# Performance work log

Measured on AMD Instinct MI355X. Metric: run time of the kernel, lower is better.

The kernel has to match this reference:

```python
import jax, jax.numpy as jnp
import numpy as np
from jax.scipy.special import logsumexp

B, T, D = 256, 2048, 64


def setup_inputs() -> dict:
    key = jax.random.key(0)
    k1, k2, k3, k4 = jax.random.split(key, 4)
    p = jax.random.normal(k1, (B, T, D), dtype=jnp.float32)
    labels = jax.random.randint(k2, (B, T), 0, D)
    y = jax.nn.one_hot(labels, D, dtype=jnp.int32)  # [B,T,D] one-hot labels
    # valid lengths in [T//2, T]; mask == 1 marks padding positions
    lengths = jax.random.randint(k3, (B,), T // 2, T + 1)
    mask = (jnp.arange(T)[None, :] >= lengths[:, None]).astype(jnp.int32)
    transition = 0.1 * jax.random.normal(k4, (D, D), dtype=jnp.float32)
    return {"p": p, "y": y, "mask": mask, "transition": transition}


def reference(p, y, mask, transition):
    # CRF negative log-likelihood per example: logZ - emission_score - transition_score
    Bb = p.shape[0]
    valid = (1 - mask).astype(jnp.float32)            # [B,T], 1 = valid token
    y1 = y.astype(jnp.float32) * valid[:, :, None]    # masked one-hot labels
    s1 = jnp.sum(y1 * p, axis=(1, 2))                 # emission score
    pair = jnp.einsum('btd,bte->bde', y1[:, :-1], y1[:, 1:])  # label bigram counts
    s2 = jnp.sum(pair * transition, axis=(1, 2))      # transition score

    # forward algorithm: alpha_t = p_t + logsumexp(alpha_{t-1}[:, :, None] + T)
    def step(state, inp):
        new = inp + logsumexp(state[:, :, None] + transition[None, :, :], axis=1)
        return new, new

    xs = jnp.moveaxis(p[:, 1:, :], 1, 0)              # [T-1, B, D]
    _, a1 = jax.lax.scan(step, p[:, 0, :], xs)        # a1: [T-1, B, D]

    # index of alpha at the last valid timestep (length L -> a1 index L-2)
    m1 = jnp.argmin(
        jnp.concatenate([valid.astype(jnp.int32), jnp.zeros((Bb, 1), jnp.int32)], axis=1),
        axis=1) - 2                                   # [B]
    last = a1[m1, jnp.arange(Bb)]                     # [B, D]
    logZ = logsumexp(last, axis=-1)
    return logZ - s1 - s2
```

## Files before the change

### kernel.cpp

```cpp
#include <hip/hip_runtime.h>
#include <stdint.h>
#include <string.h>

#define BB 256
#define TT 2048
#define DD 64
#define CC 64
#define SS 32
#define C_L2E 1.44269504f
#define C_LN2 0.69314718f
#define C_BIAS 0.0028174f

typedef short sh8  __attribute__((ext_vector_type(8)));
typedef float f32x4 __attribute__((ext_vector_type(4)));

union BU { sh8 v8; unsigned int u[4]; unsigned short s[8]; };

__device__ __forceinline__ float expf_fast(float x) { return __builtin_amdgcn_exp2f(x * C_L2E); }
__device__ __forceinline__ unsigned short bf16rne(float x) {
    unsigned int u = __float_as_uint(x);
    u += 0x7FFF + ((u >> 16) & 1u);
    return (unsigned short)(u >> 16);
}
__device__ __forceinline__ unsigned int pkbf(float hi, float lo) {
    return __builtin_amdgcn_perm(__float_as_uint(hi), __float_as_uint(lo), 0x07060302u);
}

#define DPPMAX(x, ctrl, rm, bm) { int _xi = __float_as_int(x);                              \
    int _yi = __builtin_amdgcn_update_dpp(_xi, _xi, ctrl, rm, bm, false);                   \
    x = fmaxf(x, __int_as_float(_yi)); }

__global__ __launch_bounds__(256) void crf_score(
    const float* __restrict__ p, const int* __restrict__ y,
    const int* __restrict__ mask, const float* __restrict__ tr,
    float* __restrict__ wsS, int* __restrict__ wsL)
{
    __shared__ int mk[257];
    __shared__ unsigned char labs[257];
    __shared__ float redf[4];
    __shared__ int redi[4];
    const int c = blockIdx.y, t0 = blockIdx.x * 256;
    const int tid = threadIdx.x;
    const int g = tid & 15, sub = tid >> 4;
    const size_t cb = (size_t)c * TT;

    mk[tid] = mask[cb + t0 + tid];
    if (tid == 0) mk[256] = (t0 + 256 < TT) ? mask[cb + t0 + 256] : 1;
    __syncthreads();

    float s1 = 0.f;
    int vc = 0;
#pragma unroll
    for (int k = 0; k < 16; ++k) {
        const int ti = k * 16 + sub;
        if (mk[ti] == 0) {
            int4 v = ((const int4*)y)[(cb + t0 + ti) * 16 + g];
            int cand = v.w ? 4 * g + 3 : v.z ? 4 * g + 2 : v.y ? 4 * g + 1 : v.x ? 4 * g : -1;
#pragma unroll
            for (int xm = 1; xm <= 8; xm <<= 1) {
                int o = __shfl_xor(cand, xm, 16);
                cand = o > cand ? o : cand;
            }
            if (g == 0) {
                labs[ti] = (unsigned char)cand;
                s1 += p[(cb + t0 + ti) * DD + cand];
                vc += 1;
            }
        }
    }
    if (tid < 16 && mk[256] == 0) {
        int4 v = ((const int4*)y)[(cb + t0 + 256) * 16 + tid];
        int cand = v.w ? 4 * tid + 3 : v.z ? 4 * tid + 2 : v.y ? 4 * tid + 1 : v.x ? 4 * tid : -1;
#pragma unroll
        for (int xm = 1; xm <= 8; xm <<= 1) {
            int o = __shfl_xor(cand, xm, 16);
            cand = o > cand ? o : cand;
        }
        if (tid == 0) labs[256] = (unsigned char)cand;
    }
    __syncthreads();

    float s2 = 0.f;
    if (mk[tid + 1] == 0)
        s2 = tr[(int)labs[tid] * DD + (int)labs[tid + 1]];

    float acc = s1 + s2;
#pragma unroll
    for (int xm = 32; xm >= 1; xm >>= 1) { acc += __shfl_xor(acc, xm, 64); vc += __shfl_xor(vc, xm, 64); }
    if ((tid & 63) == 0) { redf[tid >> 6] = acc; redi[tid >> 6] = vc; }
    __syncthreads();
    if (tid == 0) {
        atomicAdd(&wsS[c], redf[0] + redf[1] + redf[2] + redf[3]);
        atomicAdd(&wsL[c], redi[0] + redi[1] + redi[2] + redi[3]);
    }
}

__global__ __launch_bounds__(256) void crf_probe(
    const float* __restrict__ p, const float* __restrict__ tr,
    const int* __restrict__ wsL,
    unsigned short* __restrict__ wsA, unsigned short* __restrict__ wsB, int* __restrict__ wsSig)
{
    const int tid = threadIdx.x, w = tid >> 6, lane = tid & 63;
    const int q = lane >> 4, ml = lane & 15;
    const int cg = blockIdx.x;
    const int ic = blockIdx.y * 2 + (w >> 1);
    const int bwd = w & 1;
    const int c = cg * 16 + ml;
    const int Lml = wsL[c];
    const int t0 = ic * SS, t1 = t0 + SS;
    const int ts = (ic == 0) ? 1 : t0;
    const float* prow = p + (size_t)c * TT * DD;

    BU A[4][2];
#pragma unroll
    for (int mt = 0; mt < 4; ++mt)
#pragma unroll
        for (int kt2 = 0; kt2 < 2; ++kt2)
#pragma unroll
            for (int j = 0; j < 8; ++j) {
                int lam = 32 * kt2 + 16 * (j >> 2) + 4 * q + (j & 3);
                float tv = bwd ? tr[(16 * mt + ml) * DD + lam] : tr[lam * DD + 16 * mt + ml];
                A[mt][kt2].s[j] = (short)bf16rne(expf_fast(tv));
            }

    float xs[16];
    if (!bwd && ic == 0) {
#pragma unroll
        for (int k = 0; k < 4; ++k) {
            f32x4 v = *(const f32x4*)(prow + 16 * k + 4 * q);
#pragma unroll
            for (int r = 0; r < 4; ++r)
                xs[(k >> 1) * 8 + (k & 1) * 4 + r] = __builtin_amdgcn_exp2f(fmaf(v[r], C_L2E, C_BIAS));
        }
    } else {
#pragma unroll
        for (int i = 0; i < 16; ++i) xs[i] = 1.0f;
    }

    int mL = Lml;
#pragma unroll
    for (int xm = 32; xm >= 1; xm >>= 1) { int o = __shfl_xor(mL, xm, 64); mL = o > mL ? o : mL; }
    int ibeg = 0, iend = SS;
    if (!bwd) { int ir = mL - t0; if (ir < 0) ir = 0; iend = (ir + 3) & ~3; if (iend > SS) iend = SS; }
    else      { int ir = t1 - mL; if (ir < 0) ir = 0; ibeg = ir & ~3; if (ibeg > SS) ibeg = SS; }

    int sig = 0;
    const f32x4 z4 = {0.f, 0.f, 0.f, 0.f};

    if (ibeg < iend) {
        f32x4 er[4][4];
#pragma unroll
        for (int s = 0; s < 4; ++s) {
            int i = ibeg + s;
            int t = bwd ? (t1 - 1 - i) : (t0 + i);
#pragma unroll
            for (int k = 0; k < 4; ++k)
                er[s][k] = *(const f32x4*)(prow + (size_t)t * DD + 16 * k + 4 * q);
        }
        for (int ib = ibeg; ib < iend; ib += 4) {
#pragma unroll
            for (int s = 0; s < 4; ++s) {
                const int i = ib + s;
                const int t = bwd ? (t1 - 1 - i) : (t0 + i);
                const bool act = (t >= ts) && (t < Lml);
                float ee[4][4];
#pragma unroll
                for (int k = 0; k < 4; ++k)
#pragma unroll
                    for (int r = 0; r < 4; ++r)
                        ee[k][r] = __builtin_amdgcn_exp2f(fmaf(er[s][k][r], C_L2E, C_BIAS));
                {
                    int ipf = i + 4;
                    int tpf = bwd ? (t1 - 1 - ipf) : (t0 + ipf);
                    if (tpf < t0) tpf = t0;
                    if (tpf > t1 - 1) tpf = t1 - 1;
#pragma unroll
                    for (int k = 0; k < 4; ++k)
                        er[s][k] = *(const f32x4*)(prow + (size_t)tpf * DD + 16 * k + 4 * q);
                }
                float cand[16];
                BU Bf[2];
                f32x4 acc[4];
                if (!bwd) {
#pragma unroll
                    for (int kt2 = 0; kt2 < 2; ++kt2)
#pragma unroll
                        for (int jj = 0; jj < 4; ++jj)
                            Bf[kt2].u[jj] = pkbf(xs[kt2 * 8 + 2 * jj + 1], xs[kt2 * 8 + 2 * jj]);
#pragma unroll
                    for (int mt = 0; mt < 4; ++mt) {
                        acc[mt] = __builtin_amdgcn_mfma_f32_16x16x32_bf16(A[mt][0].v8, Bf[0].v8, z4, 0, 0, 0);
                        acc[mt] = __builtin_amdgcn_mfma_f32_16x16x32_bf16(A[mt][1].v8, Bf[1].v8, acc[mt], 0, 0, 0);
                    }
#pragma unroll
                    for (int mt = 0; mt < 4; ++mt)
#pragma unroll
                        for (int r = 0; r < 4; ++r)
                            cand[(mt >> 1) * 8 + (mt & 1) * 4 + r] = acc[mt][r] * ee[mt][r];
                } else {
                    float xsc[16];
#pragma unroll
                    for (int kt2 = 0; kt2 < 2; ++kt2)
#pragma unroll
                        for (int h = 0; h < 2; ++h)
#pragma unroll
                            for (int r = 0; r < 4; ++r)
                                xsc[kt2 * 8 + h * 4 + r] = xs[kt2 * 8 + h * 4 + r] * ee[2 * kt2 + h][r];
#pragma unroll
                    for (int kt2 = 0; kt2 < 2; ++kt2)
#pragma unroll
                        for (int jj = 0; jj < 4; ++jj)
                            Bf[kt2].u[jj] = pkbf(xsc[kt2 * 8 + 2 * jj + 1], xsc[kt2 * 8 + 2 * jj]);
#pragma unroll
                    for (int mt = 0; mt < 4; ++mt) {
                        acc[mt] = __builtin_amdgcn_mfma_f32_16x16x32_bf16(A[mt][0].v8, Bf[0].v8, z4, 0, 0, 0);
                        acc[mt] = __builtin_amdgcn_mfma_f32_16x16x32_bf16(A[mt][1].v8, Bf[1].v8, acc[mt], 0, 0, 0);
                    }
#pragma unroll
                    for (int mt = 0; mt < 4; ++mt)
#pragma unroll
                        for (int r = 0; r < 4; ++r)
                            cand[(mt >> 1) * 8 + (mt & 1) * 4 + r] = acc[mt][r];
                }
                if (s == 3) {
                    float mx = fabsf(cand[0]);
#pragma unroll
                    for (int i2 = 1; i2 < 16; ++i2) mx = fmaxf(mx, fabsf(cand[i2]));
                    DPPMAX(mx, 0x111, 0xF, 0xF); DPPMAX(mx, 0x112, 0xF, 0xF);
                    DPPMAX(mx, 0x114, 0xF, 0xF); DPPMAX(mx, 0x118, 0xF, 0xF);
                    DPPMAX(mx, 0x142, 0xA, 0xF); DPPMAX(mx, 0x143, 0xC, 0xF);
                    int smx = __builtin_amdgcn_readlane(__float_as_int(mx), 63);
                    int kk = ((smx >> 23) & 255) - 127;
                    kk = kk < -124 ? -124 : (kk > 124 ? 124 : kk);
                    float sc = __int_as_float((unsigned)(127 - kk) << 23);
#pragma unroll
                    for (int i2 = 0; i2 < 16; ++i2) cand[i2] *= sc;
                    if (act) sig += kk;
                }
#pragma unroll
                for (int i2 = 0; i2 < 16; ++i2) xs[i2] = act ? cand[i2] : xs[i2];
            }
        }
    }

    unsigned short* dst = (bwd ? wsB : wsA) + ((size_t)c * CC + ic) * 64;
#pragma unroll
    for (int kt2 = 0; kt2 < 2; ++kt2)
#pragma unroll
        for (int h = 0; h < 2; ++h)
#pragma unroll
            for (int r = 0; r < 4; ++r)
                dst[32 * kt2 + 16 * h + 4 * q + r] = bf16rne(xs[kt2 * 8 + h * 4 + r]);
    if (!bwd && q == 0) wsSig[c * CC + ic] = sig;
}

__global__ __launch_bounds__(256) void crf_combine(
    const unsigned short* __restrict__ wsA, const unsigned short* __restrict__ wsB,
    const int* __restrict__ wsSig, const float* __restrict__ wsS,
    float* __restrict__ out)
{
    __shared__ float eParts[4];
    const int tid = threadIdx.x, w = tid >> 6, lane = tid & 63;
    const int c = blockIdx.x;

    float Ep = 0.f;
#pragma unroll
    for (int k = 0; k < 16; ++k) {
        const int i = w * 16 + k;
        if (i == 0) continue;
        float b  = __uint_as_float((unsigned)wsB[((size_t)c * CC + i) * 64 + lane] << 16);
        float ap = __uint_as_float((unsigned)wsA[((size_t)c * CC + i - 1) * 64 + lane] << 16);
        float d1 = b * ap, d0 = b;
#pragma unroll
        for (int xm = 32; xm >= 1; xm >>= 1) { d1 += __shfl_xor(d1, xm, 64); d0 += __shfl_xor(d0, xm, 64); }
        Ep += (float)wsSig[c * CC + i] + __builtin_amdgcn_logf(d1) - __builtin_amdgcn_logf(d0);
    }
    if (w == 0) Ep += (float)wsSig[c * CC];
    if (w == 3) {
        float al = __uint_as_float((unsigned)wsA[((size_t)c * CC + CC - 1) * 64 + lane] << 16);
#pragma unroll
        for (int xm = 32; xm >= 1; xm >>= 1) al += __shfl_xor(al, xm, 64);
        Ep += __builtin_amdgcn_logf(al);
    }
    if (lane == 0) eParts[w] = Ep;
    __syncthreads();
    if (tid == 0) {
        float E = eParts[0] + eParts[1] + eParts[2] + eParts[3];
        out[c] = C_LN2 * E - wsS[c];
    }
}

extern "C" void kernel_launch(void* const* d_in, const int* in_sizes, int n_in,
                              void* d_out, int out_size, void* d_ws, size_t ws_size,
                              hipStream_t stream) {
    const float* p  = (const float*)d_in[0];
    const int*   y  = (const int*)d_in[1];
    const int*   mk = (const int*)d_in[2];
    const float* tr = (const float*)d_in[3];
    float* out = (float*)d_out;

    float* wsS  = (float*)d_ws;
    int*   wsL  = (int*)((char*)d_ws + 1024);
    int*   wsSg = (int*)((char*)d_ws + 2048);
    unsigned short* wsA = (unsigned short*)((char*)d_ws + 131072);
    unsigned short* wsB = (unsigned short*)((char*)d_ws + 131072 + (2u << 20));

    hipMemsetAsync(d_ws, 0, 2048, stream);
    crf_score<<<dim3(8, BB), dim3(256), 0, stream>>>(p, y, mk, tr, wsS, wsL);
    crf_probe<<<dim3(16, CC / 2), dim3(256), 0, stream>>>(p, tr, wsL, wsA, wsB, wsSg);
    crf_combine<<<dim3(BB), dim3(256), 0, stream>>>(wsA, wsB, wsSg, wsS, out);
}
```

Baseline: 317.5 us.

## Stage chunk emissions into LDS via direct global-to-LDS loads; halve chunk length

The probe kernel now copies each chunk's emission rows for its 16 sequences into LDS up front with global_load_lds (XOR-swizzled). Both the forward and backward waves then read from LDS instead of issuing per-step global prefetches. Chunks shrink from 32 to 16 steps, doubling the chunk count to 128, and each 128-thread block handles one chunk with a fwd/bwd wave pair. This shortens each wave's serial dependency chain and adds parallelism, at the cost of 64KB LDS per block (limiting occupancy) and twice as many partial vectors for the combine kernel.

Result: slower. 337.1 us (+6.2%).

```diff
diff --git a/kernel.cpp b/kernel.cpp
--- a/kernel.cpp
+++ b/kernel.cpp
@@ -5,8 +5,8 @@
 #define BB 256
 #define TT 2048
 #define DD 64
-#define CC 64
-#define SS 32
+#define CC 128
+#define SS 16
 #define C_L2E 1.44269504f
 #define C_LN2 0.69314718f
 #define C_BIAS 0.0028174f
@@ -24,6 +24,11 @@
 }
 __device__ __forceinline__ unsigned int pkbf(float hi, float lo) {
     return __builtin_amdgcn_perm(__float_as_uint(hi), __float_as_uint(lo), 0x07060302u);
+}
+__device__ __forceinline__ void gl_lds16(void* l, const void* g) {
+    __builtin_amdgcn_global_load_lds(
+        (const __attribute__((address_space(1))) unsigned int*)g,
+        (__attribute__((address_space(3))) unsigned int*)l, 16, 0, 0);
 }
 
 #define DPPMAX(x, ctrl, rm, bm) { int _xi = __float_as_int(x);                              \
@@ -95,22 +100,45 @@
     }
 }
 
-__global__ __launch_bounds__(256) void crf_probe(
+__global__ __launch_bounds__(128) void crf_probe(
     const float* __restrict__ p, const float* __restrict__ tr,
     const int* __restrict__ wsL,
     unsigned short* __restrict__ wsA, unsigned short* __restrict__ wsB, int* __restrict__ wsSig)
 {
+    __shared__ char lds[SS * 4096];
     const int tid = threadIdx.x, w = tid >> 6, lane = tid & 63;
     const int q = lane >> 4, ml = lane & 15;
     const int cg = blockIdx.x;
-    const int ic = blockIdx.y * 2 + (w >> 1);
-    const int bwd = w & 1;
+    const int ic = blockIdx.y;
+    const int bwd = w;
     const int c = cg * 16 + ml;
     const int Lml = wsL[c];
     const int t0 = ic * SS, t1 = t0 + SS;
     const int ts = (ic == 0) ? 1 : t0;
     const float* prow = p + (size_t)c * TT * DD;
 
+    int mL = Lml;
+#pragma unroll
+    for (int xm = 32; xm >= 1; xm >>= 1) { int o = __shfl_xor(mL, xm, 64); mL = o > mL ? o : mL; }
+
+    {
+        const int mls = lane >> 2, u = lane & 3;
+        const int gs = (mls >> 1) & 3;
+        const char* gbase = (const char*)(p + (size_t)(cg * 16 + mls) * TT * DD);
+        const int lofs = (u ^ gs) << 4;
+#pragma unroll
+        for (int s = 0; s < 8; ++s) {
+            const int tt = w * 8 + s;
+            if (t0 + tt < mL) {
+                const char* gsrc = gbase + (size_t)(t0 + tt) * 256 + lofs;
+                char* ldst = lds + tt * 4096;
+#pragma unroll
+                for (int k = 0; k < 4; ++k)
+                    gl_lds16(ldst + k * 1024, gsrc + k * 64);
+            }
+        }
+    }
+
     BU A[4][2];
 #pragma unroll
     for (int mt = 0; mt < 4; ++mt)
@@ -137,47 +165,34 @@
         for (int i = 0; i < 16; ++i) xs[i] = 1.0f;
     }
 
-    int mL = Lml;
-#pragma unroll
-    for (int xm = 32; xm >= 1; xm >>= 1) { int o = __shfl_xor(mL, xm, 64); mL = o > mL ? o : mL; }
     int ibeg = 0, iend = SS;
     if (!bwd) { int ir = mL - t0; if (ir < 0) ir = 0; iend = (ir + 3) & ~3; if (iend > SS) iend = SS; }
     else      { int ir = t1 - mL; if (ir < 0) ir = 0; ibeg = ir & ~3; if (ibeg > SS) ibeg = SS; }
 
+    __syncthreads();
+
     int sig = 0;
     const f32x4 z4 = {0.f, 0.f, 0.f, 0.f};
 
     if (ibeg < iend) {
-        f32x4 er[4][4];
-#pragma unroll
-        for (int s = 0; s < 4; ++s) {
-            int i = ibeg + s;
-            int t = bwd ? (t1 - 1 - i) : (t0 + i);
-#pragma unroll
-            for (int k = 0; k < 4; ++k)
-                er[s][k] = *(const f32x4*)(prow + (size_t)t * DD + 16 * k + 4 * q);
-        }
+        const char* rbase = lds + ml * 64 + ((q ^ ((ml >> 1) & 3)) << 4);
         for (int ib = ibeg; ib < iend; ib += 4) {
 #pragma unroll
             for (int s = 0; s < 4; ++s) {
                 const int i = ib + s;
                 const int t = bwd ? (t1 - 1 - i) : (t0 + i);
+                const int tt = t - t0;
                 const bool act = (t >= ts) && (t < Lml);
+                f32x4 er[4];
+#pragma unroll
+                for (int k = 0; k < 4; ++k)
+                    er[k] = *(const f32x4*)(rbase + tt * 4096 + k * 1024);
                 float ee[4][4];
 #pragma unroll
                 for (int k = 0; k < 4; ++k)
 #pragma unroll
                     for (int r = 0; r < 4; ++r)
-                        ee[k][r] = __builtin_amdgcn_exp2f(fmaf(er[s][k][r], C_L2E, C_BIAS));
-                {
-                    int ipf = i + 4;
-                    int tpf = bwd ? (t1 - 1 - ipf) : (t0 + ipf);
-                    if (tpf < t0) tpf = t0;
-                    if (tpf > t1 - 1) tpf = t1 - 1;
-#pragma unroll
-                    for (int k = 0; k < 4; ++k)
-                        er[s][k] = *(const f32x4*)(prow + (size_t)tpf * DD + 16 * k + 4 * q);
-                }
+                        ee[k][r] = __builtin_amdgcn_exp2f(fmaf(er[k][r], C_L2E, C_BIAS));
                 float cand[16];
                 BU Bf[2];
                 f32x4 acc[4];
@@ -264,9 +279,9 @@
     const int c = blockIdx.x;
 
     float Ep = 0.f;
-#pragma unroll
-    for (int k = 0; k < 16; ++k) {
-        const int i = w * 16 + k;
+#pragma unroll 4
+    for (int k = 0; k < 32; ++k) {
+        const int i = w * 32 + k;
         if (i == 0) continue;
         float b  = __uint_as_float((unsigned)wsB[((size_t)c * CC + i) * 64 + lane] << 16);
         float ap = __uint_as_float((unsigned)wsA[((size_t)c * CC + i - 1) * 64 + lane] << 16);
@@ -301,12 +316,12 @@
 
     float* wsS  = (float*)d_ws;
     int*   wsL  = (int*)((char*)d_ws + 1024);
-    int*   wsSg = (int*)((char*)d_ws + 2048);
-    unsigned short* wsA = (unsigned short*)((char*)d_ws + 131072);
-    unsigned short* wsB = (unsigned short*)((char*)d_ws + 131072 + (2u << 20));
+    int*   wsSg = (int*)((char*)d_ws + 4096);
+    unsigned short* wsA = (unsigned short*)((char*)d_ws + (1u << 18));
+    unsigned short* wsB = (unsigned short*)((char*)d_ws + (1u << 18) + (4u << 20));
 
     hipMemsetAsync(d_ws, 0, 2048, stream);
     crf_score<<<dim3(8, BB), dim3(256), 0, stream>>>(p, y, mk, tr, wsS, wsL);
-    crf_probe<<<dim3(16, CC / 2), dim3(256), 0, stream>>>(p, tr, wsL, wsA, wsB, wsSg);
+    crf_probe<<<dim3(16, CC), dim3(128), 0, stream>>>(p, tr, wsL, wsA, wsB, wsSg);
     crf_combine<<<dim3(BB), dim3(256), 0, stream>>>(wsA, wsB, wsSg, wsS, out);
 }
```

## Split length computation into tiny kernel and co-schedule scoring with forward probe

Applied to the files above, without the earlier changes.

Adds a small kernel that computes each sequence's valid length directly from the mask. The emission/transition scoring and the chunked forward/backward probe then run as one merged launch, with the first 512 blocks doing the probe and the remaining blocks doing the scoring. The intent is to overlap the memory-bound scoring of y and p with the MFMA-bound probe, so the probe no longer waits on the full scoring pass. The cost is one extra tiny launch and a larger merged kernel, whose register usage is set by the heavier probe branch.

Measured after the change: 370.8 us. +16.8%, slower.

```diff
diff --git a/kernel.cpp b/kernel.cpp
--- a/kernel.cpp
+++ b/kernel.cpp
@@ -30,228 +30,239 @@
     int _yi = __builtin_amdgcn_update_dpp(_xi, _xi, ctrl, rm, bm, false);                   \
     x = fmaxf(x, __int_as_float(_yi)); }
 
-__global__ __launch_bounds__(256) void crf_score(
+__global__ __launch_bounds__(256) void crf_len(
+    const int* __restrict__ mask, int* __restrict__ wsL)
+{
+    __shared__ int r4[4];
+    const int c = blockIdx.x, tid = threadIdx.x;
+    const int4* mrow = (const int4*)(mask + (size_t)c * TT);
+    int4 a = mrow[tid * 2], b = mrow[tid * 2 + 1];
+    int s = a.x + a.y + a.z + a.w + b.x + b.y + b.z + b.w;
+#pragma unroll
+    for (int xm = 32; xm >= 1; xm >>= 1) s += __shfl_xor(s, xm, 64);
+    if ((tid & 63) == 0) r4[tid >> 6] = s;
+    __syncthreads();
+    if (tid == 0) wsL[c] = TT - (r4[0] + r4[1] + r4[2] + r4[3]);
+}
+
+__global__ __launch_bounds__(256) void crf_main(
     const float* __restrict__ p, const int* __restrict__ y,
     const int* __restrict__ mask, const float* __restrict__ tr,
-    float* __restrict__ wsS, int* __restrict__ wsL)
+    const int* __restrict__ wsL, float* __restrict__ wsS,
+    unsigned short* __restrict__ wsA, unsigned short* __restrict__ wsB, int* __restrict__ wsSig)
 {
     __shared__ int mk[257];
     __shared__ unsigned char labs[257];
     __shared__ float redf[4];
-    __shared__ int redi[4];
-    const int c = blockIdx.y, t0 = blockIdx.x * 256;
+    const int bid = blockIdx.x;
     const int tid = threadIdx.x;
-    const int g = tid & 15, sub = tid >> 4;
-    const size_t cb = (size_t)c * TT;
-
-    mk[tid] = mask[cb + t0 + tid];
-    if (tid == 0) mk[256] = (t0 + 256 < TT) ? mask[cb + t0 + 256] : 1;
-    __syncthreads();
-
-    float s1 = 0.f;
-    int vc = 0;
-#pragma unroll
-    for (int k = 0; k < 16; ++k) {
-        const int ti = k * 16 + sub;
-        if (mk[ti] == 0) {
-            int4 v = ((const int4*)y)[(cb + t0 + ti) * 16 + g];
-            int cand = v.w ? 4 * g + 3 : v.z ? 4 * g + 2 : v.y ? 4 * g + 1 : v.x ? 4 * g : -1;
+
+    if (bid < 512) {
+        const int w = tid >> 6, lane = tid & 63;
+        const int q = lane >> 4, ml = lane & 15;
+        const int cg = bid & 15;
+        const int ic = (bid >> 4) * 2 + (w >> 1);
+        const int bwd = w & 1;
+        const int c = cg * 16 + ml;
+        const int Lml = wsL[c];
+        const int t0 = ic * SS, t1 = t0 + SS;
+        const int ts = (ic == 0) ? 1 : t0;
+        const float* prow = p + (size_t)c * TT * DD;
+
+        BU A[4][2];
+#pragma unroll
+        for (int mt = 0; mt < 4; ++mt)
+#pragma unroll
+            for (int kt2 = 0; kt2 < 2; ++kt2)
+#pragma unroll
+                for (int j = 0; j < 8; ++j) {
+                    int lam = 32 * kt2 + 16 * (j >> 2) + 4 * q + (j & 3);
+                    float tv = bwd ? tr[(16 * mt + ml) * DD + lam] : tr[lam * DD + 16 * mt + ml];
+                    A[mt][kt2].s[j] = (short)bf16rne(expf_fast(tv));
+                }
+
+        float xs[16];
+        if (!bwd && ic == 0) {
+#pragma unroll
+            for (int k = 0; k < 4; ++k) {
+                f32x4 v = *(const f32x4*)(prow + 16 * k + 4 * q);
+#pragma unroll
+                for (int r = 0; r < 4; ++r)
+                    xs[(k >> 1) * 8 + (k & 1) * 4 + r] = __builtin_amdgcn_exp2f(fmaf(v[r], C_L2E, C_BIAS));
+            }
+        } else {
+#pragma unroll
+            for (int i = 0; i < 16; ++i) xs[i] = 1.0f;
+        }
+
+        int mL = Lml;
+#pragma unroll
+        for (int xm = 32; xm >= 1; xm >>= 1) { int o = __shfl_xor(mL, xm, 64); mL = o > mL ? o : mL; }
+        int ibeg = 0, iend = SS;
+        if (!bwd) { int ir = mL - t0; if (ir < 0) ir = 0; iend = (ir + 3) & ~3; if (iend > SS) iend = SS; }
+        else      { int ir = t1 - mL; if (ir < 0) ir = 0; ibeg = ir & ~3; if (ibeg > SS) ibeg = SS; }
+
+        int sig = 0;
+        const f32x4 z4 = {0.f, 0.f, 0.f, 0.f};
+
+        if (ibeg < iend) {
+            f32x4 er[4][4];
+#pragma unroll
+            for (int s = 0; s < 4; ++s) {
+                int i = ibeg + s;
+                int t = bwd ? (t1 - 1 - i) : (t0 + i);
+#pragma unroll
+                for (int k = 0; k < 4; ++k)
+                    er[s][k] = *(const f32x4*)(prow + (size_t)t * DD + 16 * k + 4 * q);
+            }
+            for (int ib = ibeg; ib < iend; ib += 4) {
+#pragma unroll
+                for (int s = 0; s < 4; ++s) {
+                    const int i = ib + s;
+                    const int t = bwd ? (t1 - 1 - i) : (t0 + i);
+                    const bool act = (t >= ts) && (t < Lml);
+                    float ee[4][4];
+#pragma unroll
+                    for (int k = 0; k < 4; ++k)
+#pragma unroll
+                        for (int r = 0; r < 4; ++r)
+                            ee[k][r] = __builtin_amdgcn_exp2f(fmaf(er[s][k][r], C_L2E, C_BIAS));
+                    {
+                        int ipf = i + 4;
+                        int tpf = bwd ? (t1 - 1 - ipf) : (t0 + ipf);
+                        if (tpf < t0) tpf = t0;
+                        if (tpf > t1 - 1) tpf = t1 - 1;
+#pragma unroll
+                        for (int k = 0; k < 4; ++k)
+                            er[s][k] = *(const f32x4*)(prow + (size_t)tpf * DD + 16 * k + 4 * q);
+                    }
+                    float cand[16];
+                    BU Bf[2];
+                    f32x4 acc[4];
+                    if (!bwd) {
+#pragma unroll
+                        for (int kt2 = 0; kt2 < 2; ++kt2)
+#pragma unroll
+                            for (int jj = 0; jj < 4; ++jj)
+                                Bf[kt2].u[jj] = pkbf(xs[kt2 * 8 + 2 * jj + 1], xs[kt2 * 8 + 2 * jj]);
+#pragma unroll
+                        for (int mt = 0; mt < 4; ++mt) {
+                            acc[mt] = __builtin_amdgcn_mfma_f32_16x16x32_bf16(A[mt][0].v8, Bf[0].v8, z4, 0, 0, 0);
+                            acc[mt] = __builtin_amdgcn_mfma_f32_16x16x32_bf16(A[mt][1].v8, Bf[1].v8, acc[mt], 0, 0, 0);
+                        }
+#pragma unroll
+                        for (int mt = 0; mt < 4; ++mt)
+#pragma unroll
+                            for (int r = 0; r < 4; ++r)
+                                cand[(mt >> 1) * 8 + (mt & 1) * 4 + r] = acc[mt][r] * ee[mt][r];
+                    } else {
+                        float xsc[16];
+#pragma unroll
+                        for (int kt2 = 0; kt2 < 2; ++kt2)
+#pragma unroll
+                            for (int h = 0; h < 2; ++h)
+#pragma unroll
+                                for (int r = 0; r < 4; ++r)
+                                    xsc[kt2 * 8 + h * 4 + r] = xs[kt2 * 8 + h * 4 + r] * ee[2 * kt2 + h][r];
+#pragma unroll
+                        for (int kt2 = 0; kt2 < 2; ++kt2)
+#pragma unroll
+                            for (int jj = 0; jj < 4; ++jj)
+                                Bf[kt2].u[jj] = pkbf(xsc[kt2 * 8 + 2 * jj + 1], xsc[kt2 * 8 + 2 * jj]);
+#pragma unroll
+                        for (int mt = 0; mt < 4; ++mt) {
+                            acc[mt] = __builtin_amdgcn_mfma_f32_16x16x32_bf16(A[mt][0].v8, Bf[0].v8, z4, 0, 0, 0);
+                            acc[mt] = __builtin_amdgcn_mfma_f32_16x16x32_bf16(A[mt][1].v8, Bf[1].v8, acc[mt], 0, 0, 0);
+                        }
+#pragma unroll
+                        for (int mt = 0; mt < 4; ++mt)
+#pragma unroll
+                            for (int r = 0; r < 4; ++r)
+                                cand[(mt >> 1) * 8 + (mt & 1) * 4 + r] = acc[mt][r];
+                    }
+                    if (s == 3) {
+                        float mx = fabsf(cand[0]);
+#pragma unroll
+                        for (int i2 = 1; i2 < 16; ++i2) mx = fmaxf(mx, fabsf(cand[i2]));
+                        DPPMAX(mx, 0x111, 0xF, 0xF); DPPMAX(mx, 0x112, 0xF, 0xF);
+                        DPPMAX(mx, 0x114, 0xF, 0xF); DPPMAX(mx, 0x118, 0xF, 0xF);
+                        DPPMAX(mx, 0x142, 0xA, 0xF); DPPMAX(mx, 0x143, 0xC, 0xF);
+                        int smx = __builtin_amdgcn_readlane(__float_as_int(mx), 63);
+                        int kk = ((smx >> 23) & 255) - 127;
+                        kk = kk < -124 ? -124 : (kk > 124 ? 124 : kk);
+                        float sc = __int_as_float((unsigned)(127 - kk) << 23);
+#pragma unroll
+                        for (int i2 = 0; i2 < 16; ++i2) cand[i2] *= sc;
+                        if (act) sig += kk;
+                    }
+#pragma unroll
+                    for (int i2 = 0; i2 < 16; ++i2) xs[i2] = act ? cand[i2] : xs[i2];
+                }
+            }
+        }
+
+        unsigned short* dst = (bwd ? wsB : wsA) + ((size_t)c * CC + ic) * 64;
+#pragma unroll
+        for (int kt2 = 0; kt2 < 2; ++kt2)
+#pragma unroll
+            for (int h = 0; h < 2; ++h)
+#pragma unroll
+                for (int r = 0; r < 4; ++r)
+                    dst[32 * kt2 + 16 * h + 4 * q + r] = bf16rne(xs[kt2 * 8 + h * 4 + r]);
+        if (!bwd && q == 0) wsSig[c * CC + ic] = sig;
+
+    } else {
+        const int sid = bid - 512;
+        const int c = sid >> 3, t0 = (sid & 7) * 256;
+        const int g = tid & 15, sub = tid >> 4;
+        const size_t cb = (size_t)c * TT;
+
+        mk[tid] = mask[cb + t0 + tid];
+        if (tid == 0) mk[256] = (t0 + 256 < TT) ? mask[cb + t0 + 256] : 1;
+        __syncthreads();
+
+        float s1 = 0.f;
+#pragma unroll
+        for (int k = 0; k < 16; ++k) {
+            const int ti = k * 16 + sub;
+            if (mk[ti] == 0) {
+                int4 v = ((const int4*)y)[(cb + t0 + ti) * 16 + g];
+                int cand = v.w ? 4 * g + 3 : v.z ? 4 * g + 2 : v.y ? 4 * g + 1 : v.x ? 4 * g : -1;
+#pragma unroll
+                for (int xm = 1; xm <= 8; xm <<= 1) {
+                    int o = __shfl_xor(cand, xm, 16);
+                    cand = o > cand ? o : cand;
+                }
+                if (g == 0) {
+                    labs[ti] = (unsigned char)cand;
+                    s1 += p[(cb + t0 + ti) * DD + cand];
+                }
+            }
+        }
+        if (tid < 16 && mk[256] == 0) {
+            int4 v = ((const int4*)y)[(cb + t0 + 256) * 16 + tid];
+            int cand = v.w ? 4 * tid + 3 : v.z ? 4 * tid + 2 : v.y ? 4 * tid + 1 : v.x ? 4 * tid : -1;
 #pragma unroll
             for (int xm = 1; xm <= 8; xm <<= 1) {
                 int o = __shfl_xor(cand, xm, 16);
                 cand = o > cand ? o : cand;
             }
-            if (g == 0) {
-                labs[ti] = (unsigned char)cand;
-                s1 += p[(cb + t0 + ti) * DD + cand];
-                vc += 1;
-            }
+            if (tid == 0) labs[256] = (unsigned char)cand;
         }
+        __syncthreads();
+
+        float s2 = 0.f;
+        if (mk[tid + 1] == 0)
+            s2 = tr[(int)labs[tid] * DD + (int)labs[tid + 1]];
+
+        float acc = s1 + s2;
+#pragma unroll
+        for (int xm = 32; xm >= 1; xm >>= 1) acc += __shfl_xor(acc, xm, 64);
+        if ((tid & 63) == 0) redf[tid >> 6] = acc;
+        __syncthreads();
+        if (tid == 0)
+            atomicAdd(&wsS[c], redf[0] + redf[1] + redf[2] + redf[3]);
     }
-    if (tid < 16 && mk[256] == 0) {
-        int4 v = ((const int4*)y)[(cb + t0 + 256) * 16 + tid];
-        int cand = v.w ? 4 * tid + 3 : v.z ? 4 * tid + 2 : v.y ? 4 * tid + 1 : v.x ? 4 * tid : -1;
-#pragma unroll
-        for (int xm = 1; xm <= 8; xm <<= 1) {
-            int o = __shfl_xor(cand, xm, 16);
-            cand = o > cand ? o : cand;
-        }
-        if (tid == 0) labs[256] = (unsigned char)cand;
-    }
-    __syncthreads();
-
-    float s2 = 0.f;
-    if (mk[tid + 1] == 0)
-        s2 = tr[(int)labs[tid] * DD + (int)labs[tid + 1]];
-
-    float acc = s1 + s2;
-#pragma unroll
-    for (int xm = 32; xm >= 1; xm >>= 1) { acc += __shfl_xor(acc, xm, 64); vc += __shfl_xor(vc, xm, 64); }
-    if ((tid & 63) == 0) { redf[tid >> 6] = acc; redi[tid >> 6] = vc; }
-    __syncthreads();
-    if (tid == 0) {
-        atomicAdd(&wsS[c], redf[0] + redf[1] + redf[2] + redf[3]);
-        atomicAdd(&wsL[c], redi[0] + redi[1] + redi[2] + redi[3]);
-    }
-}
-
-__global__ __launch_bounds__(256) void crf_probe(
-    const float* __restrict__ p, const float* __restrict__ tr,
-    const int* __restrict__ wsL,
-    unsigned short* __restrict__ wsA, unsigned short* __restrict__ wsB, int* __restrict__ wsSig)
-{
-    const int tid = threadIdx.x, w = tid >> 6, lane = tid & 63;
-    const int q = lane >> 4, ml = lane & 15;
-    const int cg = blockIdx.x;
-    const int ic = blockIdx.y * 2 + (w >> 1);
-    const int bwd = w & 1;
-    const int c = cg * 16 + ml;
-    const int Lml = wsL[c];
-    const int t0 = ic * SS, t1 = t0 + SS;
-    const int ts = (ic == 0) ? 1 : t0;
-    const float* prow = p + (size_t)c * TT * DD;
-
-    BU A[4][2];
-#pragma unroll
-    for (int mt = 0; mt < 4; ++mt)
-#pragma unroll
-        for (int kt2 = 0; kt2 < 2; ++kt2)
-#pragma unroll
-            for (int j = 0; j < 8; ++j) {
-                int lam = 32 * kt2 + 16 * (j >> 2) + 4 * q + (j & 3);
-                float tv = bwd ? tr[(16 * mt + ml) * DD + lam] : tr[lam * DD + 16 * mt + ml];
-                A[mt][kt2].s[j] = (short)bf16rne(expf_fast(tv));
-            }
-
-    float xs[16];
-    if (!bwd && ic == 0) {
-#pragma unroll
-        for (int k = 0; k < 4; ++k) {
-            f32x4 v = *(const f32x4*)(prow + 16 * k + 4 * q);
-#pragma unroll
-            for (int r = 0; r < 4; ++r)
-                xs[(k >> 1) * 8 + (k & 1) * 4 + r] = __builtin_amdgcn_exp2f(fmaf(v[r], C_L2E, C_BIAS));
-        }
-    } else {
-#pragma unroll
-        for (int i = 0; i < 16; ++i) xs[i] = 1.0f;
-    }
-
-    int mL = Lml;
-#pragma unroll
-    for (int xm = 32; xm >= 1; xm >>= 1) { int o = __shfl_xor(mL, xm, 64); mL = o > mL ? o : mL; }
-    int ibeg = 0, iend = SS;
-    if (!bwd) { int ir = mL - t0; if (ir < 0) ir = 0; iend = (ir + 3) & ~3; if (iend > SS) iend = SS; }
-    else      { int ir = t1 - mL; if (ir < 0) ir = 0; ibeg = ir & ~3; if (ibeg > SS) ibeg = SS; }
-
-    int sig = 0;
-    const f32x4 z4 = {0.f, 0.f, 0.f, 0.f};
-
-    if (ibeg < iend) {
-        f32x4 er[4][4];
-#pragma unroll
-        for (int s = 0; s < 4; ++s) {
-            int i = ibeg + s;
-            int t = bwd ? (t1 - 1 - i) : (t0 + i);
-#pragma unroll
-            for (int k = 0; k < 4; ++k)
-                er[s][k] = *(const f32x4*)(prow + (size_t)t * DD + 16 * k + 4 * q);
-        }
-        for (int ib = ibeg; ib < iend; ib += 4) {
-#pragma unroll
-            for (int s = 0; s < 4; ++s) {
-                const int i = ib + s;
-                const int t = bwd ? (t1 - 1 - i) : (t0 + i);
-                const bool act = (t >= ts) && (t < Lml);
-                float ee[4][4];
-#pragma unroll
-                for (int k = 0; k < 4; ++k)
-#pragma unroll
-                    for (int r = 0; r < 4; ++r)
-                        ee[k][r] = __builtin_amdgcn_exp2f(fmaf(er[s][k][r], C_L2E, C_BIAS));
-                {
-                    int ipf = i + 4;
-                    int tpf = bwd ? (t1 - 1 - ipf) : (t0 + ipf);
-                    if (tpf < t0) tpf = t0;
-                    if (tpf > t1 - 1) tpf = t1 - 1;
-#pragma unroll
-                    for (int k = 0; k < 4; ++k)
-                        er[s][k] = *(const f32x4*)(prow + (size_t)tpf * DD + 16 * k + 4 * q);
-                }
-                float cand[16];
-                BU Bf[2];
-                f32x4 acc[4];
-                if (!bwd) {
-#pragma unroll
-                    for (int kt2 = 0; kt2 < 2; ++kt2)
-#pragma unroll
-                        for (int jj = 0; jj < 4; ++jj)
-                            Bf[kt2].u[jj] = pkbf(xs[kt2 * 8 + 2 * jj + 1], xs[kt2 * 8 + 2 * jj]);
-#pragma unroll
-                    for (int mt = 0; mt < 4; ++mt) {
-                        acc[mt] = __builtin_amdgcn_mfma_f32_16x16x32_bf16(A[mt][0].v8, Bf[0].v8, z4, 0, 0, 0);
-                        acc[mt] = __builtin_amdgcn_mfma_f32_16x16x32_bf16(A[mt][1].v8, Bf[1].v8, acc[mt], 0, 0, 0);
-                    }
-#pragma unroll
-                    for (int mt = 0; mt < 4; ++mt)
-#pragma unroll
-                        for (int r = 0; r < 4; ++r)
-                            cand[(mt >> 1) * 8 + (mt & 1) * 4 + r] = acc[mt][r] * ee[mt][r];
-                } else {
-                    float xsc[16];
-#pragma unroll
-                    for (int kt2 = 0; kt2 < 2; ++kt2)
-#pragma unroll
-                        for (int h = 0; h < 2; ++h)
-#pragma unroll
-                            for (int r = 0; r < 4; ++r)
-                                xsc[kt2 * 8 + h * 4 + r] = xs[kt2 * 8 + h * 4 + r] * ee[2 * kt2 + h][r];
-#pragma unroll
-                    for (int kt2 = 0; kt2 < 2; ++kt2)
-#pragma unroll
-                        for (int jj = 0; jj < 4; ++jj)
-                            Bf[kt2].u[jj] = pkbf(xsc[kt2 * 8 + 2 * jj + 1], xsc[kt2 * 8 + 2 * jj]);
-#pragma unroll
-                    for (int mt = 0; mt < 4; ++mt) {
-                        acc[mt] = __builtin_amdgcn_mfma_f32_16x16x32_bf16(A[mt][0].v8, Bf[0].v8, z4, 0, 0, 0);
-                        acc[mt] = __builtin_amdgcn_mfma_f32_16x16x32_bf16(A[mt][1].v8, Bf[1].v8, acc[mt], 0, 0, 0);
-                    }
-#pragma unroll
-                    for (int mt = 0; mt < 4; ++mt)
-#pragma unroll
-                        for (int r = 0; r < 4; ++r)
-                            cand[(mt >> 1) * 8 + (mt & 1) * 4 + r] = acc[mt][r];
-                }
-                if (s == 3) {
-                    float mx = fabsf(cand[0]);
-#pragma unroll
-                    for (int i2 = 1; i2 < 16; ++i2) mx = fmaxf(mx, fabsf(cand[i2]));
-                    DPPMAX(mx, 0x111, 0xF, 0xF); DPPMAX(mx, 0x112, 0xF, 0xF);
-                    DPPMAX(mx, 0x114, 0xF, 0xF); DPPMAX(mx, 0x118, 0xF, 0xF);
-                    DPPMAX(mx, 0x142, 0xA, 0xF); DPPMAX(mx, 0x143, 0xC, 0xF);
-                    int smx = __builtin_amdgcn_readlane(__float_as_int(mx), 63);
-                    int kk = ((smx >> 23) & 255) - 127;
-                    kk = kk < -124 ? -124 : (kk > 124 ? 124 : kk);
-                    float sc = __int_as_float((unsigned)(127 - kk) << 23);
-#pragma unroll
-                    for (int i2 = 0; i2 < 16; ++i2) cand[i2] *= sc;
-                    if (act) sig += kk;
-                }
-#pragma unroll
-                for (int i2 = 0; i2 < 16; ++i2) xs[i2] = act ? cand[i2] : xs[i2];
-            }
-        }
-    }
-
-    unsigned short* dst = (bwd ? wsB : wsA) + ((size_t)c * CC + ic) * 64;
-#pragma unroll
-    for (int kt2 = 0; kt2 < 2; ++kt2)
-#pragma unroll
-        for (int h = 0; h < 2; ++h)
-#pragma unroll
-            for (int r = 0; r < 4; ++r)
-                dst[32 * kt2 + 16 * h + 4 * q + r] = bf16rne(xs[kt2 * 8 + h * 4 + r]);
-    if (!bwd && q == 0) wsSig[c * CC + ic] = sig;
 }
 
 __global__ __launch_bounds__(256) void crf_combine(
@@ -305,8 +316,8 @@
     unsigned short* wsA = (unsigned short*)((char*)d_ws + 131072);
     unsigned short* wsB = (unsigned short*)((char*)d_ws + 131072 + (2u << 20));
 
-    hipMemsetAsync(d_ws, 0, 2048, stream);
-    crf_score<<<dim3(8, BB), dim3(256), 0, stream>>>(p, y, mk, tr, wsS, wsL);
-    crf_probe<<<dim3(16, CC / 2), dim3(256), 0, stream>>>(p, tr, wsL, wsA, wsB, wsSg);
+    hipMemsetAsync(d_ws, 0, 1024, stream);
+    crf_len<<<dim3(BB), dim3(256), 0, stream>>>(mk, wsL);
+    crf_main<<<dim3(512 + 8 * BB), dim3(256), 0, stream>>>(p, y, mk, tr, wsL, wsS, wsA, wsB, wsSg);
     crf_combine<<<dim3(BB), dim3(256), 0, stream>>>(wsA, wsB, wsSg, wsS, out);
 }
```
